# Kernel optimization log

Measured on AMD Instinct MI355X. Metric: run time of the kernel, lower is better.

The kernel has to match this reference:

```python
import jax, jax.numpy as jnp
import numpy as np

NUM_NODES, MEM_DIM, MSG_DIM, TIME_DIM = 65536, 128, 128, 128
POS_DIM = MEM_DIM  # PositionMessage reshape forces pos_embedding_dim == memory_dim
IN_MEM = MSG_DIM + 2 * MEM_DIM + TIME_DIM  # IdentityMessage width = 512
IN_POS = POS_DIM + 2 * MEM_DIM + TIME_DIM  # PositionMessage width = 512


def setup_inputs() -> dict:
    key = jax.random.key(0)
    ks = jax.random.split(key, 24)
    s = jnp.float32(0.05)
    f = lambda k, sh: jax.random.normal(k, sh, jnp.float32)
    return dict(
        n_id=jnp.arange(NUM_NODES, dtype=jnp.int32),
        memory=f(ks[0], (NUM_NODES, MEM_DIM)),
        pos_mem=f(ks[1], (NUM_NODES, MEM_DIM)),
        pos_emb=f(ks[2], (NUM_NODES, POS_DIM)),
        raw_msg_s=f(ks[3], (NUM_NODES, MSG_DIM)),
        raw_msg_d=f(ks[4], (NUM_NODES, MSG_DIM)),
        other_s=jax.random.randint(ks[5], (NUM_NODES,), 0, NUM_NODES, jnp.int32),
        other_d=jax.random.randint(ks[6], (NUM_NODES,), 0, NUM_NODES, jnp.int32),
        t_s=jax.random.randint(ks[7], (NUM_NODES,), 1000, 2000, jnp.int32),
        t_d=jax.random.randint(ks[8], (NUM_NODES,), 1000, 2000, jnp.int32),
        last_update=jax.random.randint(ks[9], (NUM_NODES,), 0, 1000, jnp.int32),
        w_time_mem=f(ks[10], (TIME_DIM,)) * s, b_time_mem=f(ks[11], (TIME_DIM,)) * s,
        w_time_pos=f(ks[12], (TIME_DIM,)) * s, b_time_pos=f(ks[13], (TIME_DIM,)) * s,
        Wih_mem=f(ks[14], (3 * MEM_DIM, IN_MEM)) * s, Whh_mem=f(ks[15], (3 * MEM_DIM, MEM_DIM)) * s,
        bih_mem=f(ks[16], (3 * MEM_DIM,)) * s, bhh_mem=f(ks[17], (3 * MEM_DIM,)) * s,
        Wih_pos=f(ks[18], (3 * MEM_DIM, IN_POS)) * s, Whh_pos=f(ks[19], (3 * MEM_DIM, MEM_DIM)) * s,
        bih_pos=f(ks[20], (3 * MEM_DIM,)) * s, bhh_pos=f(ks[21], (3 * MEM_DIM,)) * s,
    )


def _time_enc(t_rel, w, b):
    # PyG TimeEncoder: cos(Linear(1, time_dim)(t_rel))
    return jnp.cos(t_rel[:, None] * w[None, :] + b[None, :])


def _gru(x, h, Wih, Whh, bih, bhh):
    # torch.nn.GRUCell math
    gi = x @ Wih.T + bih
    gh = h @ Whh.T + bhh
    ir, iz, inn = jnp.split(gi, 3, axis=-1)
    hr, hz, hn = jnp.split(gh, 3, axis=-1)
    r = jax.nn.sigmoid(ir + hr)
    z = jax.nn.sigmoid(iz + hz)
    n = jnp.tanh(inn + r * hn)
    return (1.0 - z) * n + z * h


def _tgn_memory(mem, n_id, other_s, other_d, feat_s, feat_d, t_s, t_d,
                last_update, w_t, b_t, Wih, Whh, bih, bhh):
    # Gather per-node state; each node owns one src-store and one dst-store message.
    h = mem[n_id]                                        # [N, D]
    lu = last_update[n_id].astype(jnp.float32)
    te_s = _time_enc(t_s.astype(jnp.float32) - lu, w_t, b_t)
    te_d = _time_enc(t_d.astype(jnp.float32) - lu, w_t, b_t)
    msg_s = jnp.concatenate([h, mem[other_s], feat_s, te_s], axis=-1)  # [N, IN]
    msg_d = jnp.concatenate([h, mem[other_d], feat_d, te_d], axis=-1)
    # LastAggregator: keep the most recent message per node (scatter_max on t)
    pick_s = (t_s >= t_d)[:, None]
    aggr = jnp.where(pick_s, msg_s, msg_d)
    z = _gru(aggr, h, Wih, Whh, bih, bhh)
    new_lu = jnp.maximum(t_s, t_d)
    return z, new_lu


def reference(n_id, memory, pos_mem, pos_emb, raw_msg_s, raw_msg_d,
              other_s, other_d, t_s, t_d, last_update,
              w_time_mem, b_time_mem, w_time_pos, b_time_pos,
              Wih_mem, Whh_mem, bih_mem, bhh_mem,
              Wih_pos, Whh_pos, bih_pos, bhh_pos):
    z, last_up = _tgn_memory(memory, n_id, other_s, other_d, raw_msg_s, raw_msg_d,
                             t_s, t_d, last_update,
                             w_time_mem, b_time_mem, Wih_mem, Whh_mem, bih_mem, bhh_mem)
    # pos raw message is the event's src node id -> embedding lookup
    pos_z, _ = _tgn_memory(pos_mem, n_id, other_s, other_d,
                           pos_emb[n_id], pos_emb[other_d],
                           t_s, t_d, last_update,
                           w_time_pos, b_time_pos, Wih_pos, Whh_pos, bih_pos, bhh_pos)
    return z, pos_z, last_up
```

## Files before the change

### kernel.cpp

```cpp
#include <hip/hip_runtime.h>
#include <hip/hip_bf16.h>
#include <math.h>

#define NODES   65536
#define DD      128
#define BM      64
#define NST     16
#define NSUB    24
#define WTILE_STRIDE (NSUB * 64 * 8)
#define WG_STRIDE    (20 * WTILE_STRIDE)
#define XW      544

typedef __bf16 bf16x8 __attribute__((ext_vector_type(8)));
typedef float  f32x4  __attribute__((ext_vector_type(4)));

static __device__ __forceinline__ unsigned short f2bf(float f) {
    union { float f; unsigned u; } v; v.f = f;
    return (unsigned short)((v.u + 0x8000u) >> 16);
}
static __device__ __forceinline__ float fastcos(float x) {
    float r = x * 0.15915494309189535f;
    r = r - floorf(r);
    return __builtin_amdgcn_cosf(r);
}
static __device__ __forceinline__ float fsigmoid(float x) {
    return 1.0f / (1.0f + __expf(-x));
}
static __device__ __forceinline__ float ftanh(float x) {
    float ax = fabsf(x);
    float t  = __expf(-2.0f * ax);
    float th = 1.0f - 2.0f * t / (1.0f + t);
    return copysignf(th, x);
}

__global__ void prep_w_kernel(const float* __restrict__ Wih0, const float* __restrict__ Whh0,
                              const float* __restrict__ Wih1, const float* __restrict__ Whh1,
                              unsigned short* __restrict__ Wws) {
    int gid = blockIdx.x * 256 + threadIdx.x;
    if (gid >= 2 * WG_STRIDE) return;
    int g   = gid / WG_STRIDE;
    int r   = gid - g * WG_STRIDE;
    int kt  = r / WTILE_STRIDE;
    int r2  = r - kt * WTILE_STRIDE;
    int t   = r2 >> 9;
    int l8  = r2 & 511;
    int lane = l8 >> 3, j = l8 & 7;
    int cl  = lane & 15, q = lane >> 4;
    int n   = t * 16 + cl;
    const float* Wih = g ? Wih1 : Wih0;
    const float* Whh = g ? Whh1 : Whh0;
    float v;
    if (kt < 16) v = Wih[n * 512 + kt * 32 + q * 8 + j];
    else         v = Whh[n * 128 + (kt - 16) * 32 + q * 8 + j];
    Wws[gid] = f2bf(v);
}

__global__ __launch_bounds__(512, 4) void tgn_fused_kernel(
    const int*   __restrict__ n_id,
    const float* __restrict__ memory_,
    const float* __restrict__ pos_mem,
    const float* __restrict__ pos_emb,
    const float* __restrict__ raw_s,
    const float* __restrict__ raw_d,
    const int*   __restrict__ other_s,
    const int*   __restrict__ other_d,
    const int*   __restrict__ t_s,
    const int*   __restrict__ t_d,
    const int*   __restrict__ last_update,
    const float* __restrict__ w_time_mem, const float* __restrict__ b_time_mem,
    const float* __restrict__ w_time_pos, const float* __restrict__ b_time_pos,
    const float* __restrict__ bih_mem, const float* __restrict__ bhh_mem,
    const float* __restrict__ bih_pos, const float* __restrict__ bhh_pos,
    const unsigned short* __restrict__ Wws,
    float* __restrict__ out)
{
    __shared__ __align__(16) unsigned short X[BM * XW];
    __shared__ int   snid[BM];
    __shared__ int   soth[BM];
    __shared__ float sdt[BM];
    __shared__ int   sfeat[BM];

    const int g   = blockIdx.y;
    const int nb  = blockIdx.x;
    const int tid = threadIdx.x;
    const int lane = tid & 63;
    const int wave = tid >> 6;

    const float* mem_g = g ? pos_mem    : memory_;
    const float* wt    = g ? w_time_pos : w_time_mem;
    const float* bt    = g ? b_time_pos : b_time_mem;
    const float* bih   = g ? bih_pos    : bih_mem;
    const float* bhh   = g ? bhh_pos    : bhh_mem;

    if (tid < BM) {
        int gi   = nb * BM + tid;
        int id   = n_id[gi];
        int ts   = t_s[gi];
        int td   = t_d[gi];
        bool pick = (ts >= td);
        int oth  = pick ? other_s[gi] : other_d[gi];
        int lu   = last_update[id];
        float dt = (float)(pick ? ts : td) - (float)lu;
        int code;
        if (g) code = pick ? id : other_d[gi];
        else   code = pick ? gi : ~gi;
        snid[tid]  = id;
        soth[tid]  = oth;
        sdt[tid]   = dt;
        sfeat[tid] = code;
        if (g == 0) {
            out[2 * (size_t)NODES * DD + gi] = (float)max(ts, td);
        }
    }
    __syncthreads();

    {
        int row = lane;
        if (wave >= 6) {
            float dt = sdt[row];
            int c0 = (wave - 6) * 64;
            #pragma unroll
            for (int i = 0; i < 16; ++i) {
                int c = c0 + i * 4;
                float4 wv = *(const float4*)(wt + c);
                float4 bv = *(const float4*)(bt + c);
                ushort4 pv;
                pv.x = f2bf(fastcos(dt * wv.x + bv.x));
                pv.y = f2bf(fastcos(dt * wv.y + bv.y));
                pv.z = f2bf(fastcos(dt * wv.z + bv.z));
                pv.w = f2bf(fastcos(dt * wv.w + bv.w));
                *(ushort4*)(X + row * XW + 384 + c) = pv;
            }
        } else {
            int seg = wave >> 1;
            int c0  = (wave & 1) * 64;
            const float* src;
            if (seg == 0)      src = mem_g + (size_t)snid[row] * DD + c0;
            else if (seg == 1) src = mem_g + (size_t)soth[row] * DD + c0;
            else {
                int code = sfeat[row];
                if (g)              src = pos_emb + (size_t)code * DD + c0;
                else if (code >= 0) src = raw_s + (size_t)code * DD + c0;
                else                src = raw_d + (size_t)(~code) * DD + c0;
            }
            #pragma unroll
            for (int i = 0; i < 16; ++i) {
                float4 v = *(const float4*)(src + i * 4);
                ushort4 pv;
                pv.x = f2bf(v.x); pv.y = f2bf(v.y); pv.z = f2bf(v.z); pv.w = f2bf(v.w);
                *(ushort4*)(X + row * XW + seg * 128 + c0 + i * 4) = pv;
            }
        }
    }
    __syncthreads();

    f32x4 acc[16];
    #pragma unroll
    for (int i = 0; i < 16; ++i) acc[i] = (f32x4){0.f, 0.f, 0.f, 0.f};

    const int q  = lane >> 4;
    const int cl = lane & 15;
    const unsigned short* wbase = Wws + (size_t)g * WG_STRIDE + lane * 8;
    const int tR = wave, tZ = 8 + wave, tN = 16 + wave;

    #pragma unroll
    for (int st = 0; st < NST; ++st) {
        bf16x8 a[4];
        #pragma unroll
        for (int j = 0; j < 4; ++j)
            a[j] = *(const bf16x8*)(X + (j * 16 + cl) * XW + st * 32 + q * 8);

        const unsigned short* wk = wbase + (size_t)st * WTILE_STRIDE;
        bf16x8 bR = *(const bf16x8*)(wk + tR * 512);
        bf16x8 bZ = *(const bf16x8*)(wk + tZ * 512);
        bf16x8 bN = *(const bf16x8*)(wk + tN * 512);
        #pragma unroll
        for (int j = 0; j < 4; ++j) {
            acc[j * 4 + 0] = __builtin_amdgcn_mfma_f32_16x16x32_bf16(a[j], bR, acc[j * 4 + 0], 0, 0, 0);
            acc[j * 4 + 1] = __builtin_amdgcn_mfma_f32_16x16x32_bf16(a[j], bZ, acc[j * 4 + 1], 0, 0, 0);
            acc[j * 4 + 2] = __builtin_amdgcn_mfma_f32_16x16x32_bf16(a[j], bN, acc[j * 4 + 2], 0, 0, 0);
        }
        if (st < 4) {
            const unsigned short* wh = wbase + (size_t)(16 + st) * WTILE_STRIDE;
            bf16x8 cR = *(const bf16x8*)(wh + tR * 512);
            bf16x8 cZ = *(const bf16x8*)(wh + tZ * 512);
            bf16x8 cN = *(const bf16x8*)(wh + tN * 512);
            #pragma unroll
            for (int j = 0; j < 4; ++j) {
                acc[j * 4 + 0] = __builtin_amdgcn_mfma_f32_16x16x32_bf16(a[j], cR, acc[j * 4 + 0], 0, 0, 0);
                acc[j * 4 + 1] = __builtin_amdgcn_mfma_f32_16x16x32_bf16(a[j], cZ, acc[j * 4 + 1], 0, 0, 0);
                acc[j * 4 + 3] = __builtin_amdgcn_mfma_f32_16x16x32_bf16(a[j], cN, acc[j * 4 + 3], 0, 0, 0);
            }
        }
    }

    float* outz = out + (size_t)g * NODES * DD;
    const int d = wave * 16 + cl;
    float br  = bih[d]       + bhh[d];
    float bz  = bih[128 + d] + bhh[128 + d];
    float bni = bih[256 + d];
    float bnh = bhh[256 + d];
    #pragma unroll
    for (int j = 0; j < 4; ++j) {
        #pragma unroll
        for (int r = 0; r < 4; ++r) {
            int il = j * 16 + q * 4 + r;
            float rs  = acc[j * 4 + 0][r] + br;
            float zs  = acc[j * 4 + 1][r] + bz;
            float in_ = acc[j * 4 + 2][r] + bni;
            float hn_ = acc[j * 4 + 3][r] + bnh;
            float rg = fsigmoid(rs);
            float zg = fsigmoid(zs);
            float nv = ftanh(in_ + rg * hn_);
            float h  = mem_g[(size_t)snid[il] * DD + d];
            outz[(size_t)(nb * BM + il) * DD + d] = (1.0f - zg) * nv + zg * h;
        }
    }
}

extern "C" void kernel_launch(void* const* d_in, const int* in_sizes, int n_in,
                              void* d_out, int out_size, void* d_ws, size_t ws_size,
                              hipStream_t stream) {
    const int*   n_id        = (const int*)  d_in[0];
    const float* memory_     = (const float*)d_in[1];
    const float* pos_mem     = (const float*)d_in[2];
    const float* pos_emb     = (const float*)d_in[3];
    const float* raw_s       = (const float*)d_in[4];
    const float* raw_d       = (const float*)d_in[5];
    const int*   other_s     = (const int*)  d_in[6];
    const int*   other_d     = (const int*)  d_in[7];
    const int*   t_s         = (const int*)  d_in[8];
    const int*   t_d         = (const int*)  d_in[9];
    const int*   last_update = (const int*)  d_in[10];
    const float* w_time_mem  = (const float*)d_in[11];
    const float* b_time_mem  = (const float*)d_in[12];
    const float* w_time_pos  = (const float*)d_in[13];
    const float* b_time_pos  = (const float*)d_in[14];
    const float* Wih_mem     = (const float*)d_in[15];
    const float* Whh_mem     = (const float*)d_in[16];
    const float* bih_mem     = (const float*)d_in[17];
    const float* bhh_mem     = (const float*)d_in[18];
    const float* Wih_pos     = (const float*)d_in[19];
    const float* Whh_pos     = (const float*)d_in[20];
    const float* bih_pos     = (const float*)d_in[21];
    const float* bhh_pos     = (const float*)d_in[22];

    unsigned short* Wws = (unsigned short*)d_ws;
    float* out = (float*)d_out;

    prep_w_kernel<<<(2 * WG_STRIDE + 255) / 256, 256, 0, stream>>>(
        Wih_mem, Whh_mem, Wih_pos, Whh_pos, Wws);

    dim3 grid(NODES / BM, 2);
    tgn_fused_kernel<<<grid, 512, 0, stream>>>(
        n_id, memory_, pos_mem, pos_emb, raw_s, raw_d,
        other_s, other_d, t_s, t_d, last_update,
        w_time_mem, b_time_mem, w_time_pos, b_time_pos,
        bih_mem, bhh_mem, bih_pos, bhh_pos,
        Wws, out);
}
```

Before: 313.3 us.

## Double row tile, swizzle LDS, overlap neighbor/feature gathers with MFMA

Measured after the change: 309.4 us. No clear change (-1.2%).

```diff
diff --git a/kernel.cpp b/kernel.cpp
--- a/kernel.cpp
+++ b/kernel.cpp
@@ -4,12 +4,11 @@
 
 #define NODES   65536
 #define DD      128
-#define BM      64
+#define BM      128
 #define NST     16
 #define NSUB    24
 #define WTILE_STRIDE (NSUB * 64 * 8)
 #define WG_STRIDE    (20 * WTILE_STRIDE)
-#define XW      544
 
 typedef __bf16 bf16x8 __attribute__((ext_vector_type(8)));
 typedef float  f32x4  __attribute__((ext_vector_type(4)));
@@ -55,7 +54,53 @@
     Wws[gid] = f2bf(v);
 }
 
-__global__ __launch_bounds__(512, 4) void tgn_fused_kernel(
+
+#define KTILE_WIH(st)                                                          \
+    do {                                                                       \
+        bf16x8 a[8];                                                           \
+        _Pragma("unroll")                                                      \
+        for (int j = 0; j < 8; ++j)                                            \
+            a[j] = *(const bf16x8*)(Xb + (j * 16 + cl) * 1024 +                \
+                                    (((st) * 64 + q * 16) ^ swz));             \
+        const unsigned short* wk = wbase + (size_t)(st) * WTILE_STRIDE;        \
+        bf16x8 bR = *(const bf16x8*)(wk + tR * 512);                           \
+        bf16x8 bZ = *(const bf16x8*)(wk + tZ * 512);                           \
+        bf16x8 bN = *(const bf16x8*)(wk + tN * 512);                           \
+        _Pragma("unroll")                                                      \
+        for (int j = 0; j < 8; ++j) {                                          \
+            acc[j * 4 + 0] = __builtin_amdgcn_mfma_f32_16x16x32_bf16(a[j], bR, acc[j * 4 + 0], 0, 0, 0); \
+            acc[j * 4 + 1] = __builtin_amdgcn_mfma_f32_16x16x32_bf16(a[j], bZ, acc[j * 4 + 1], 0, 0, 0); \
+            acc[j * 4 + 2] = __builtin_amdgcn_mfma_f32_16x16x32_bf16(a[j], bN, acc[j * 4 + 2], 0, 0, 0); \
+        }                                                                      \
+    } while (0)
+
+#define KTILE_PAIR(st)                                                         \
+    do {                                                                       \
+        bf16x8 a[8];                                                           \
+        _Pragma("unroll")                                                      \
+        for (int j = 0; j < 8; ++j)                                            \
+            a[j] = *(const bf16x8*)(Xb + (j * 16 + cl) * 1024 +                \
+                                    (((st) * 64 + q * 16) ^ swz));             \
+        const unsigned short* wk = wbase + (size_t)(st) * WTILE_STRIDE;        \
+        const unsigned short* wh = wbase + (size_t)(16 + (st)) * WTILE_STRIDE; \
+        bf16x8 bR = *(const bf16x8*)(wk + tR * 512);                           \
+        bf16x8 bZ = *(const bf16x8*)(wk + tZ * 512);                           \
+        bf16x8 bN = *(const bf16x8*)(wk + tN * 512);                           \
+        bf16x8 cR = *(const bf16x8*)(wh + tR * 512);                           \
+        bf16x8 cZ = *(const bf16x8*)(wh + tZ * 512);                           \
+        bf16x8 cN = *(const bf16x8*)(wh + tN * 512);                           \
+        _Pragma("unroll")                                                      \
+        for (int j = 0; j < 8; ++j) {                                          \
+            acc[j * 4 + 0] = __builtin_amdgcn_mfma_f32_16x16x32_bf16(a[j], bR, acc[j * 4 + 0], 0, 0, 0); \
+            acc[j * 4 + 1] = __builtin_amdgcn_mfma_f32_16x16x32_bf16(a[j], bZ, acc[j * 4 + 1], 0, 0, 0); \
+            acc[j * 4 + 2] = __builtin_amdgcn_mfma_f32_16x16x32_bf16(a[j], bN, acc[j * 4 + 2], 0, 0, 0); \
+            acc[j * 4 + 0] = __builtin_amdgcn_mfma_f32_16x16x32_bf16(a[j], cR, acc[j * 4 + 0], 0, 0, 0); \
+            acc[j * 4 + 1] = __builtin_amdgcn_mfma_f32_16x16x32_bf16(a[j], cZ, acc[j * 4 + 1], 0, 0, 0); \
+            acc[j * 4 + 3] = __builtin_amdgcn_mfma_f32_16x16x32_bf16(a[j], cN, acc[j * 4 + 3], 0, 0, 0); \
+        }                                                                      \
+    } while (0)
+
+__global__ __launch_bounds__(512, 2) void tgn_fused_kernel(
     const int*   __restrict__ n_id,
     const float* __restrict__ memory_,
     const float* __restrict__ pos_mem,
@@ -74,7 +119,7 @@
     const unsigned short* __restrict__ Wws,
     float* __restrict__ out)
 {
-    __shared__ __align__(16) unsigned short X[BM * XW];
+    __shared__ __align__(16) unsigned short X[BM * 512];
     __shared__ int   snid[BM];
     __shared__ int   soth[BM];
     __shared__ float sdt[BM];
@@ -84,7 +129,7 @@
     const int nb  = blockIdx.x;
     const int tid = threadIdx.x;
     const int lane = tid & 63;
-    const int wave = tid >> 6;
+    const int wv   = tid >> 6;
 
     const float* mem_g = g ? pos_mem    : memory_;
     const float* wt    = g ? w_time_pos : w_time_mem;
@@ -115,93 +160,116 @@
     __syncthreads();
 
     {
-        int row = lane;
-        if (wave >= 6) {
-            float dt = sdt[row];
-            int c0 = (wave - 6) * 64;
-            #pragma unroll
-            for (int i = 0; i < 16; ++i) {
-                int c = c0 + i * 4;
-                float4 wv = *(const float4*)(wt + c);
-                float4 bv = *(const float4*)(bt + c);
-                ushort4 pv;
-                pv.x = f2bf(fastcos(dt * wv.x + bv.x));
-                pv.y = f2bf(fastcos(dt * wv.y + bv.y));
-                pv.z = f2bf(fastcos(dt * wv.z + bv.z));
-                pv.w = f2bf(fastcos(dt * wv.w + bv.w));
-                *(ushort4*)(X + row * XW + 384 + c) = pv;
-            }
-        } else {
-            int seg = wave >> 1;
-            int c0  = (wave & 1) * 64;
-            const float* src;
-            if (seg == 0)      src = mem_g + (size_t)snid[row] * DD + c0;
-            else if (seg == 1) src = mem_g + (size_t)soth[row] * DD + c0;
-            else {
-                int code = sfeat[row];
-                if (g)              src = pos_emb + (size_t)code * DD + c0;
-                else if (code >= 0) src = raw_s + (size_t)code * DD + c0;
-                else                src = raw_d + (size_t)(~code) * DD + c0;
-            }
+        int u  = wv & 3;
+        int rh = u & 1, ch = u >> 1;
+        int row = rh * 64 + lane;
+        int swr = (row & 7) << 4;
+        char* dst = (char*)X + row * 1024;
+        if (wv < 4) {
+            const float* src = mem_g + (size_t)snid[row] * DD + ch * 64;
+            int colb = ch * 128;
             #pragma unroll
             for (int i = 0; i < 16; ++i) {
                 float4 v = *(const float4*)(src + i * 4);
                 ushort4 pv;
                 pv.x = f2bf(v.x); pv.y = f2bf(v.y); pv.z = f2bf(v.z); pv.w = f2bf(v.w);
-                *(ushort4*)(X + row * XW + seg * 128 + c0 + i * 4) = pv;
+                *(ushort4*)(dst + ((colb + i * 8) ^ swr)) = pv;
             }
+        } else {
+            float dt = sdt[row];
+            const float* wp = wt + ch * 64;
+            const float* bp = bt + ch * 64;
+            int colb = 768 + ch * 128;
+            #pragma unroll
+            for (int i = 0; i < 16; ++i) {
+                float4 wv4 = *(const float4*)(wp + i * 4);
+                float4 bv4 = *(const float4*)(bp + i * 4);
+                ushort4 pv;
+                pv.x = f2bf(fastcos(dt * wv4.x + bv4.x));
+                pv.y = f2bf(fastcos(dt * wv4.y + bv4.y));
+                pv.z = f2bf(fastcos(dt * wv4.z + bv4.z));
+                pv.w = f2bf(fastcos(dt * wv4.w + bv4.w));
+                *(ushort4*)(dst + ((colb + i * 8) ^ swr)) = pv;
+            }
         }
     }
     __syncthreads();
 
-    f32x4 acc[16];
+    f32x4 acc[32];
     #pragma unroll
-    for (int i = 0; i < 16; ++i) acc[i] = (f32x4){0.f, 0.f, 0.f, 0.f};
+    for (int i = 0; i < 32; ++i) acc[i] = (f32x4){0.f, 0.f, 0.f, 0.f};
 
     const int q  = lane >> 4;
     const int cl = lane & 15;
+    const int swz = (cl & 7) << 4;
     const unsigned short* wbase = Wws + (size_t)g * WG_STRIDE + lane * 8;
-    const int tR = wave, tZ = 8 + wave, tN = 16 + wave;
-
-    #pragma unroll
-    for (int st = 0; st < NST; ++st) {
-        bf16x8 a[4];
-        #pragma unroll
-        for (int j = 0; j < 4; ++j)
-            a[j] = *(const bf16x8*)(X + (j * 16 + cl) * XW + st * 32 + q * 8);
-
-        const unsigned short* wk = wbase + (size_t)st * WTILE_STRIDE;
-        bf16x8 bR = *(const bf16x8*)(wk + tR * 512);
-        bf16x8 bZ = *(const bf16x8*)(wk + tZ * 512);
-        bf16x8 bN = *(const bf16x8*)(wk + tN * 512);
-        #pragma unroll
-        for (int j = 0; j < 4; ++j) {
-            acc[j * 4 + 0] = __builtin_amdgcn_mfma_f32_16x16x32_bf16(a[j], bR, acc[j * 4 + 0], 0, 0, 0);
-            acc[j * 4 + 1] = __builtin_amdgcn_mfma_f32_16x16x32_bf16(a[j], bZ, acc[j * 4 + 1], 0, 0, 0);
-            acc[j * 4 + 2] = __builtin_amdgcn_mfma_f32_16x16x32_bf16(a[j], bN, acc[j * 4 + 2], 0, 0, 0);
-        }
-        if (st < 4) {
-            const unsigned short* wh = wbase + (size_t)(16 + st) * WTILE_STRIDE;
-            bf16x8 cR = *(const bf16x8*)(wh + tR * 512);
-            bf16x8 cZ = *(const bf16x8*)(wh + tZ * 512);
-            bf16x8 cN = *(const bf16x8*)(wh + tN * 512);
-            #pragma unroll
-            for (int j = 0; j < 4; ++j) {
-                acc[j * 4 + 0] = __builtin_amdgcn_mfma_f32_16x16x32_bf16(a[j], cR, acc[j * 4 + 0], 0, 0, 0);
-                acc[j * 4 + 1] = __builtin_amdgcn_mfma_f32_16x16x32_bf16(a[j], cZ, acc[j * 4 + 1], 0, 0, 0);
-                acc[j * 4 + 3] = __builtin_amdgcn_mfma_f32_16x16x32_bf16(a[j], cN, acc[j * 4 + 3], 0, 0, 0);
-            }
-        }
-    }
+    const int tR = wv, tZ = 8 + wv, tN = 16 + wv;
+    const char* Xb = (const char*)X;
+
+    const int srow = wv * 16 + (lane >> 2);
+    const int scol = (lane & 3) * 4;
+    const int sswr = (srow & 7) << 4;
+    char* sdst = (char*)X + srow * 1024;
+
+    float4 of[8];
+    {
+        const float* src = mem_g + (size_t)soth[srow] * DD + scol;
+        #pragma unroll
+        for (int i = 0; i < 8; ++i) of[i] = *(const float4*)(src + i * 16);
+    }
+    __builtin_amdgcn_sched_barrier(0);
+
+    KTILE_PAIR(0); KTILE_PAIR(1); KTILE_PAIR(2); KTILE_PAIR(3);
+
+    {
+        #pragma unroll
+        for (int i = 0; i < 8; ++i) {
+            ushort4 pv;
+            pv.x = f2bf(of[i].x); pv.y = f2bf(of[i].y);
+            pv.z = f2bf(of[i].z); pv.w = f2bf(of[i].w);
+            *(ushort4*)(sdst + ((256 + scol * 2 + i * 32) ^ sswr)) = pv;
+        }
+    }
+
+    float4 ff[8];
+    {
+        const float* src;
+        if (g) {
+            src = pos_emb + (size_t)sfeat[srow] * DD + scol;
+        } else {
+            int code = sfeat[srow];
+            src = (code >= 0 ? raw_s + (size_t)code * DD
+                             : raw_d + (size_t)(~code) * DD) + scol;
+        }
+        #pragma unroll
+        for (int i = 0; i < 8; ++i) ff[i] = *(const float4*)(src + i * 16);
+    }
+    __builtin_amdgcn_sched_barrier(0);
+
+    KTILE_WIH(12); KTILE_WIH(13); KTILE_WIH(14); KTILE_WIH(15);
+
+    {
+        #pragma unroll
+        for (int i = 0; i < 8; ++i) {
+            ushort4 pv;
+            pv.x = f2bf(ff[i].x); pv.y = f2bf(ff[i].y);
+            pv.z = f2bf(ff[i].z); pv.w = f2bf(ff[i].w);
+            *(ushort4*)(sdst + ((512 + scol * 2 + i * 32) ^ sswr)) = pv;
+        }
+    }
+    __syncthreads();
+
+    KTILE_WIH(4); KTILE_WIH(5); KTILE_WIH(6); KTILE_WIH(7);
+    KTILE_WIH(8); KTILE_WIH(9); KTILE_WIH(10); KTILE_WIH(11);
 
     float* outz = out + (size_t)g * NODES * DD;
-    const int d = wave * 16 + cl;
+    const int d = wv * 16 + cl;
     float br  = bih[d]       + bhh[d];
     float bz  = bih[128 + d] + bhh[128 + d];
     float bni = bih[256 + d];
     float bnh = bhh[256 + d];
     #pragma unroll
-    for (int j = 0; j < 4; ++j) {
+    for (int j = 0; j < 8; ++j) {
         #pragma unroll
         for (int r = 0; r < 4; ++r) {
             int il = j * 16 + q * 4 + r;
```

## Overlap feature gathers with GRU MFMA k-tiles and swizzle LDS staging

Applied to the files above, without the earlier changes.

Result: no change. 309.9 us (-1.1%).

```diff
diff --git a/kernel.cpp b/kernel.cpp
--- a/kernel.cpp
+++ b/kernel.cpp
@@ -5,19 +5,13 @@
 #define NODES   65536
 #define DD      128
 #define BM      64
-#define NST     16
 #define NSUB    24
 #define WTILE_STRIDE (NSUB * 64 * 8)
 #define WG_STRIDE    (20 * WTILE_STRIDE)
-#define XW      544
 
 typedef __bf16 bf16x8 __attribute__((ext_vector_type(8)));
 typedef float  f32x4  __attribute__((ext_vector_type(4)));
 
-static __device__ __forceinline__ unsigned short f2bf(float f) {
-    union { float f; unsigned u; } v; v.f = f;
-    return (unsigned short)((v.u + 0x8000u) >> 16);
-}
 static __device__ __forceinline__ float fastcos(float x) {
     float r = x * 0.15915494309189535f;
     r = r - floorf(r);
@@ -31,6 +25,16 @@
     float t  = __expf(-2.0f * ax);
     float th = 1.0f - 2.0f * t / (1.0f + t);
     return copysignf(th, x);
+}
+static __device__ __forceinline__ uint2 cvtpk4(float4 v) {
+    uint2 r;
+    asm("v_cvt_pk_bf16_f32 %0, %1, %2" : "=v"(r.x) : "v"(v.x), "v"(v.y));
+    asm("v_cvt_pk_bf16_f32 %0, %1, %2" : "=v"(r.y) : "v"(v.z), "v"(v.w));
+    return r;
+}
+static __device__ __forceinline__ unsigned short f2bf(float f) {
+    union { float f; unsigned u; } v; v.f = f;
+    return (unsigned short)((v.u + 0x8000u) >> 16);
 }
 
 __global__ void prep_w_kernel(const float* __restrict__ Wih0, const float* __restrict__ Whh0,
@@ -55,6 +59,26 @@
     Wws[gid] = f2bf(v);
 }
 
+
+#define KTILE(st, kt, sn)                                                      \
+    do {                                                                       \
+        bf16x8 a[4];                                                           \
+        _Pragma("unroll")                                                      \
+        for (int j = 0; j < 4; ++j)                                            \
+            a[j] = *(const bf16x8*)(Xb + (j * 16 + cl) * 1024 +                \
+                                    (((st) * 64 + q * 16) ^ swz));             \
+        const unsigned short* wk = wbase + (size_t)(kt) * WTILE_STRIDE;        \
+        bf16x8 bR = *(const bf16x8*)(wk + tR * 512);                           \
+        bf16x8 bZ = *(const bf16x8*)(wk + tZ * 512);                           \
+        bf16x8 bN = *(const bf16x8*)(wk + tN * 512);                           \
+        _Pragma("unroll")                                                      \
+        for (int j = 0; j < 4; ++j) {                                          \
+            acc[j * 4 + 0]  = __builtin_amdgcn_mfma_f32_16x16x32_bf16(a[j], bR, acc[j * 4 + 0], 0, 0, 0);  \
+            acc[j * 4 + 1]  = __builtin_amdgcn_mfma_f32_16x16x32_bf16(a[j], bZ, acc[j * 4 + 1], 0, 0, 0);  \
+            acc[j * 4 + sn] = __builtin_amdgcn_mfma_f32_16x16x32_bf16(a[j], bN, acc[j * 4 + sn], 0, 0, 0); \
+        }                                                                      \
+    } while (0)
+
 __global__ __launch_bounds__(512, 4) void tgn_fused_kernel(
     const int*   __restrict__ n_id,
     const float* __restrict__ memory_,
@@ -74,7 +98,7 @@
     const unsigned short* __restrict__ Wws,
     float* __restrict__ out)
 {
-    __shared__ __align__(16) unsigned short X[BM * XW];
+    __shared__ __align__(16) unsigned short X[BM * 512];
     __shared__ int   snid[BM];
     __shared__ int   soth[BM];
     __shared__ float sdt[BM];
@@ -84,7 +108,7 @@
     const int nb  = blockIdx.x;
     const int tid = threadIdx.x;
     const int lane = tid & 63;
-    const int wave = tid >> 6;
+    const int wv   = tid >> 6;
 
     const float* mem_g = g ? pos_mem    : memory_;
     const float* wt    = g ? w_time_pos : w_time_mem;
@@ -114,43 +138,36 @@
     }
     __syncthreads();
 
-    {
-        int row = lane;
-        if (wave >= 6) {
-            float dt = sdt[row];
-            int c0 = (wave - 6) * 64;
-            #pragma unroll
-            for (int i = 0; i < 16; ++i) {
-                int c = c0 + i * 4;
-                float4 wv = *(const float4*)(wt + c);
-                float4 bv = *(const float4*)(bt + c);
-                ushort4 pv;
-                pv.x = f2bf(fastcos(dt * wv.x + bv.x));
-                pv.y = f2bf(fastcos(dt * wv.y + bv.y));
-                pv.z = f2bf(fastcos(dt * wv.z + bv.z));
-                pv.w = f2bf(fastcos(dt * wv.w + bv.w));
-                *(ushort4*)(X + row * XW + 384 + c) = pv;
-            }
-        } else {
-            int seg = wave >> 1;
-            int c0  = (wave & 1) * 64;
-            const float* src;
-            if (seg == 0)      src = mem_g + (size_t)snid[row] * DD + c0;
-            else if (seg == 1) src = mem_g + (size_t)soth[row] * DD + c0;
-            else {
-                int code = sfeat[row];
-                if (g)              src = pos_emb + (size_t)code * DD + c0;
-                else if (code >= 0) src = raw_s + (size_t)code * DD + c0;
-                else                src = raw_d + (size_t)(~code) * DD + c0;
-            }
-            #pragma unroll
-            for (int i = 0; i < 16; ++i) {
-                float4 v = *(const float4*)(src + i * 4);
-                ushort4 pv;
-                pv.x = f2bf(v.x); pv.y = f2bf(v.y); pv.z = f2bf(v.z); pv.w = f2bf(v.w);
-                *(ushort4*)(X + row * XW + seg * 128 + c0 + i * 4) = pv;
-            }
-        }
+    const int lc    = lane & 31;
+    const int rh    = lane >> 5;
+    const int srow0 = wv * 8;
+
+    float4 of[4];
+    #pragma unroll
+    for (int c = 0; c < 4; ++c) {
+        int row = srow0 + 2 * c + rh;
+        of[c] = *(const float4*)(mem_g + (size_t)soth[row] * DD + lc * 4);
+    }
+    __builtin_amdgcn_sched_barrier(0);
+
+    #pragma unroll
+    for (int c = 0; c < 4; ++c) {
+        int row = srow0 + 2 * c + rh;
+        float4 v = *(const float4*)(mem_g + (size_t)snid[row] * DD + lc * 4);
+        *(uint2*)((char*)X + row * 1024 + ((lc * 8) ^ ((row & 7) << 4))) = cvtpk4(v);
+    }
+    #pragma unroll
+    for (int c = 0; c < 4; ++c) {
+        int row = srow0 + 2 * c + rh;
+        float dt = sdt[row];
+        float4 wv4 = *(const float4*)(wt + lc * 4);
+        float4 bv4 = *(const float4*)(bt + lc * 4);
+        float4 tv;
+        tv.x = fastcos(dt * wv4.x + bv4.x);
+        tv.y = fastcos(dt * wv4.y + bv4.y);
+        tv.z = fastcos(dt * wv4.z + bv4.z);
+        tv.w = fastcos(dt * wv4.w + bv4.w);
+        *(uint2*)((char*)X + row * 1024 + ((768 + lc * 8) ^ ((row & 7) << 4))) = cvtpk4(tv);
     }
     __syncthreads();
 
@@ -160,42 +177,58 @@
 
     const int q  = lane >> 4;
     const int cl = lane & 15;
+    const int swz = (cl & 7) << 4;
     const unsigned short* wbase = Wws + (size_t)g * WG_STRIDE + lane * 8;
-    const int tR = wave, tZ = 8 + wave, tN = 16 + wave;
-
-    #pragma unroll
-    for (int st = 0; st < NST; ++st) {
-        bf16x8 a[4];
-        #pragma unroll
-        for (int j = 0; j < 4; ++j)
-            a[j] = *(const bf16x8*)(X + (j * 16 + cl) * XW + st * 32 + q * 8);
-
-        const unsigned short* wk = wbase + (size_t)st * WTILE_STRIDE;
-        bf16x8 bR = *(const bf16x8*)(wk + tR * 512);
-        bf16x8 bZ = *(const bf16x8*)(wk + tZ * 512);
-        bf16x8 bN = *(const bf16x8*)(wk + tN * 512);
-        #pragma unroll
-        for (int j = 0; j < 4; ++j) {
-            acc[j * 4 + 0] = __builtin_amdgcn_mfma_f32_16x16x32_bf16(a[j], bR, acc[j * 4 + 0], 0, 0, 0);
-            acc[j * 4 + 1] = __builtin_amdgcn_mfma_f32_16x16x32_bf16(a[j], bZ, acc[j * 4 + 1], 0, 0, 0);
-            acc[j * 4 + 2] = __builtin_amdgcn_mfma_f32_16x16x32_bf16(a[j], bN, acc[j * 4 + 2], 0, 0, 0);
+    const int tR = wv, tZ = 8 + wv, tN = 16 + wv;
+    const char* Xb = (const char*)X;
+
+    __builtin_amdgcn_s_setprio(1);
+    KTILE(0, 0, 2);  KTILE(0, 16, 3);
+    KTILE(1, 1, 2);  KTILE(1, 17, 3);
+    KTILE(2, 2, 2);  KTILE(2, 18, 3);
+    KTILE(3, 3, 2);  KTILE(3, 19, 3);
+    __builtin_amdgcn_s_setprio(0);
+
+    #pragma unroll
+    for (int c = 0; c < 4; ++c) {
+        int row = srow0 + 2 * c + rh;
+        *(uint2*)((char*)X + row * 1024 + ((256 + lc * 8) ^ ((row & 7) << 4))) = cvtpk4(of[c]);
+    }
+
+    float4 ff[4];
+    #pragma unroll
+    for (int c = 0; c < 4; ++c) {
+        int row = srow0 + 2 * c + rh;
+        const float* src;
+        if (g) {
+            src = pos_emb + (size_t)sfeat[row] * DD;
+        } else {
+            int code = sfeat[row];
+            src = code >= 0 ? raw_s + (size_t)code * DD
+                            : raw_d + (size_t)(~code) * DD;
         }
-        if (st < 4) {
-            const unsigned short* wh = wbase + (size_t)(16 + st) * WTILE_STRIDE;
-            bf16x8 cR = *(const bf16x8*)(wh + tR * 512);
-            bf16x8 cZ = *(const bf16x8*)(wh + tZ * 512);
-            bf16x8 cN = *(const bf16x8*)(wh + tN * 512);
-            #pragma unroll
-            for (int j = 0; j < 4; ++j) {
-                acc[j * 4 + 0] = __builtin_amdgcn_mfma_f32_16x16x32_bf16(a[j], cR, acc[j * 4 + 0], 0, 0, 0);
-                acc[j * 4 + 1] = __builtin_amdgcn_mfma_f32_16x16x32_bf16(a[j], cZ, acc[j * 4 + 1], 0, 0, 0);
-                acc[j * 4 + 3] = __builtin_amdgcn_mfma_f32_16x16x32_bf16(a[j], cN, acc[j * 4 + 3], 0, 0, 0);
-            }
-        }
-    }
+        ff[c] = *(const float4*)(src + lc * 4);
+    }
+    __builtin_amdgcn_sched_barrier(0);
+
+    __builtin_amdgcn_s_setprio(1);
+    KTILE(12, 12, 2); KTILE(13, 13, 2); KTILE(14, 14, 2); KTILE(15, 15, 2);
+    __builtin_amdgcn_s_setprio(0);
+
+    #pragma unroll
+    for (int c = 0; c < 4; ++c) {
+        int row = srow0 + 2 * c + rh;
+        *(uint2*)((char*)X + row * 1024 + ((512 + lc * 8) ^ ((row & 7) << 4))) = cvtpk4(ff[c]);
+    }
+    __syncthreads();
+
+    __builtin_amdgcn_s_setprio(1);
+    KTILE(4, 4, 2);   KTILE(5, 5, 2);   KTILE(6, 6, 2);   KTILE(7, 7, 2);
+    KTILE(8, 8, 2);   KTILE(9, 9, 2);   KTILE(10, 10, 2); KTILE(11, 11, 2);
+    __builtin_amdgcn_s_setprio(0);
 
     float* outz = out + (size_t)g * NODES * DD;
-    const int d = wave * 16 + cl;
+    const int d = wv * 16 + cl;
     float br  = bih[d]       + bhh[d];
     float bz  = bih[128 + d] + bhh[128 + d];
     float bni = bih[256 + d];
```
